# Kernel tuning notes

Measured on AMD Instinct MI355X. Metric: run time of the kernel, lower is better.

## Reference

```python
import jax, jax.numpy as jnp
import numpy as np

B, NBLK, D, DY, NDIM, NMC, DH = 4096, 12, 2, 2, 24, 256, 100
SQRT3 = 3.0 ** 0.5
G2 = np.array([[1.0, 0.0], [0.5, SQRT3 / 2.0]], dtype=np.float32)
G = jnp.asarray(np.kron(np.eye(NBLK, dtype=np.float32), G2))  # (24,24) block-diag hexagonal generator
LOG_VOL = (NDIM // 2) * float(np.log(SQRT3 / 2.0))  # log sqrt(det(G G^T))


def _lin(x, w, b=None):
    y = x @ w.T
    return y if b is None else y + b


def _hex_quantize(y):
    # Exact nearest-point quantizer for the product-of-A2 (hexagonal) lattice.
    p = y.reshape(y.shape[:-1] + (NDIM // 2, 2))
    off = jnp.array([0.5, SQRT3 / 2.0], dtype=y.dtype)
    def rnd(q):  # round to rectangular sublattice Z x sqrt(3)Z
        return jnp.stack([jnp.round(q[..., 0]), jnp.round(q[..., 1] / SQRT3) * SQRT3], axis=-1)
    c0 = rnd(p)
    c1 = rnd(p - off) + off
    d0 = jnp.sum((p - c0) ** 2, axis=-1)
    d1 = jnp.sum((p - c1) ** 2, axis=-1)
    return jnp.where((d0 <= d1)[..., None], c0, c1).reshape(y.shape)


def _logits_cumulative(v, Hs, bs, fs):
    # compressai-style per-channel monotone cumulative network. v: (..., C) -> (..., C)
    v = v[..., None]  # (..., C, 1)
    for k in range(len(Hs)):
        v = jnp.einsum('coi,...ci->...co', jax.nn.softplus(Hs[k]), v) + bs[k][:, :, 0]
        if k < len(fs):
            v = v + jnp.tanh(fs[k][:, :, 0]) * jnp.tanh(v)
    return v[..., 0]


def setup_inputs() -> dict:
    key = jax.random.key(0)
    ks = iter(jax.random.split(key, 64))
    def nrm(shape, s=1.0):
        return jax.random.normal(next(ks), shape, jnp.float32) * s
    inp = {}
    inp['x'] = nrm((B, NBLK, D))
    inp['y_mean'] = nrm((NBLK, DY))
    inp['u'] = jax.random.uniform(next(ks), (NMC, NDIM), jnp.float32)
    inp['ga_w0'] = nrm((DH, D), D ** -0.5); inp['ga_b0'] = jnp.zeros((DH,), jnp.float32)
    inp['ga_w1'] = nrm((DH, DH), DH ** -0.5); inp['ga_b1'] = jnp.zeros((DH,), jnp.float32)
    inp['ga_w2'] = nrm((DY, DH), DH ** -0.5); inp['ga_b2'] = jnp.zeros((DY,), jnp.float32)
    inp['gs_w0'] = nrm((DH, DY), DY ** -0.5); inp['gs_b0'] = jnp.zeros((DH,), jnp.float32)
    inp['gs_w1'] = nrm((DH, DH), DH ** -0.5); inp['gs_b1'] = jnp.zeros((DH,), jnp.float32)
    inp['gs_w2'] = nrm((D, DH), DH ** -0.5); inp['gs_b2'] = jnp.zeros((D,), jnp.float32)
    inp['gac_w0'] = nrm((DH, NDIM), NDIM ** -0.5)
    inp['gac_w1'] = nrm((DH, DH), DH ** -0.5)
    inp['gac_w2'] = nrm((NDIM, DH), DH ** -0.5)
    inp['gsc_w0'] = nrm((DH, NDIM), NDIM ** -0.5)
    inp['gsc_w1'] = nrm((DH, DH), DH ** -0.5)
    inp['gsc_w2'] = nrm((NDIM, DH), DH ** -0.5)
    # factorized-prior cumulative params, layer dims 1->3->3->3->3->1
    inp['eb_H0'] = nrm((NDIM, 3, 1), 0.5)
    inp['eb_H1'] = nrm((NDIM, 3, 3), 0.5)
    inp['eb_H2'] = nrm((NDIM, 3, 3), 0.5)
    inp['eb_H3'] = nrm((NDIM, 3, 3), 0.5)
    inp['eb_H4'] = nrm((NDIM, 1, 3), 0.5)
    inp['eb_b0'] = nrm((NDIM, 3, 1), 0.5)
    inp['eb_b1'] = nrm((NDIM, 3, 1), 0.5)
    inp['eb_b2'] = nrm((NDIM, 3, 1), 0.5)
    inp['eb_b3'] = nrm((NDIM, 3, 1), 0.5)
    inp['eb_b4'] = nrm((NDIM, 1, 1), 0.5)
    inp['eb_a0'] = nrm((NDIM, 3, 1), 0.5)
    inp['eb_a1'] = nrm((NDIM, 3, 1), 0.5)
    inp['eb_a2'] = nrm((NDIM, 3, 1), 0.5)
    inp['eb_a3'] = nrm((NDIM, 3, 1), 0.5)
    return inp


def reference(x, y_mean, u, ga_w0, ga_b0, ga_w1, ga_b1, ga_w2, ga_b2,
              gs_w0, gs_b0, gs_w1, gs_b1, gs_w2, gs_b2,
              gac_w0, gac_w1, gac_w2, gsc_w0, gsc_w1, gsc_w2,
              eb_H0, eb_H1, eb_H2, eb_H3, eb_H4,
              eb_b0, eb_b1, eb_b2, eb_b3, eb_b4,
              eb_a0, eb_a1, eb_a2, eb_a3):
    lrelu, sp = jax.nn.leaky_relu, jax.nn.softplus
    # analysis transform g_a: (B, 12, 2) -> (B, 12, dy)
    y1 = _lin(lrelu(_lin(lrelu(_lin(x, ga_w0, ga_b0)), ga_w1, ga_b1)), ga_w2, ga_b2)
    # EMA zero-mean update (buffer assignment => no gradient through the mean)
    ym = jax.lax.stop_gradient(0.05 * y_mean + 0.95 * jnp.mean(y1, axis=0))
    y1 = (y1 - ym).reshape(B, NDIM)
    # coupled analysis transform g_a_c (Softplus MLP, no bias)
    y1 = _lin(sp(_lin(sp(_lin(y1, gac_w0)), gac_w1)), gac_w2)
    # quasi-uniform samples from the Voronoi cell of the lattice origin
    u2 = u @ G
    u2 = u2 - _hex_quantize(u2)
    # lattice quantization with straight-through estimator
    y_q = _hex_quantize(y1)
    y_hat = y1 + jax.lax.stop_gradient(y_q - y1)
    # Monte-Carlo log-likelihood over the Voronoi cell with factorized prior density
    Hs = (eb_H0, eb_H1, eb_H2, eb_H3, eb_H4)
    bs = (eb_b0, eb_b1, eb_b2, eb_b3, eb_b4)
    fs = (eb_a0, eb_a1, eb_a2, eb_a3)
    pts = y_hat[:, None, :] + u2[None, :, :]  # (B, NMC, NDIM)
    def cdf(p):
        return jax.nn.sigmoid(_logits_cumulative(p, Hs, bs, fs))
    _, pdf = jax.jvp(cdf, (pts,), (jnp.ones_like(pts),))  # density = d/dx cdf(x)
    logp = jnp.sum(jnp.log(pdf + 1e-9), axis=-1)  # (B, NMC)
    lik = jax.scipy.special.logsumexp(logp, axis=1) - jnp.log(jnp.float32(NMC)) + LOG_VOL  # (B,)
    # synthesis transforms
    y_hat1 = _lin(sp(_lin(sp(_lin(y_hat, gsc_w0)), gsc_w1)), gsc_w2).reshape(B, NBLK, DY) + ym
    x_hat = _lin(lrelu(_lin(lrelu(_lin(y_hat1, gs_w0, gs_b0)), gs_w1, gs_b1)), gs_w2, gs_b2)
    return (x_hat, lik)
```

## Files before the change

kernel.cpp:

```cpp
#include <hip/hip_runtime.h>
#include <hip/hip_bf16.h>
#include <math.h>
#include <limits.h>

constexpr int NB    = 4096;
constexpr int ROWS2 = NB * 12;
constexpr int GA_BLOCKS = ROWS2 / 128;
constexpr int TBL_CAP = 64;
constexpr int KBASE   = -32;

constexpr size_t WS_Y1    = 0;
constexpr size_t WS_YHAT  = 98304;
constexpr size_t WS_YHAT1 = 196608;
constexpr size_t WS_YM    = 294912;
constexpr size_t WS_U2T   = 294936;
constexpr size_t WS_EB    = 301080;
constexpr size_t WS_PART  = 302472;
constexpr size_t WS_W1T   = 320904;
constexpr size_t WS_TBL   = 372104;
constexpr size_t WS_END   = WS_TBL + 24 * TBL_CAP * 256;

constexpr float STEP_ODD = 0.8660254037844386f;
constexpr float INV_ODD  = 1.1547005383792517f;

__device__ __forceinline__ float lrelu(float x) { return x >= 0.f ? x : 0.01f * x; }
__device__ __forceinline__ float rcp_fast(float x) { return __builtin_amdgcn_rcpf(x); }

__device__ __forceinline__ float tanh_fast(float x) {
    float xx = fminf(fmaxf(x, -15.f), 15.f);
    float e = __expf(xx + xx);
    return fmaf(-2.f, rcp_fast(e + 1.f), 1.f);
}
__device__ __forceinline__ float splus(float x) {
    return fmaxf(x, 0.f) + __logf(1.f + __expf(-fabsf(x)));
}
__device__ __forceinline__ float splus_precise(float x) {
    return fmaxf(x, 0.f) + log1pf(expf(-fabsf(x)));
}

__device__ __forceinline__ void fma4(float4& a, float h, const float4& w) {
    a.x = fmaf(h, w.x, a.x); a.y = fmaf(h, w.y, a.y);
    a.z = fmaf(h, w.z, a.z); a.w = fmaf(h, w.w, a.w);
}

__device__ __forceinline__ void hexq(float p0, float p1, float& q0, float& q1) {
    const float S3 = 1.7320508075688772f;
    const float H3 = 0.8660254037844386f;
    float c00 = rintf(p0);
    float c01 = rintf(p1 / S3) * S3;
    float c10 = rintf(p0 - 0.5f) + 0.5f;
    float c11 = rintf((p1 - H3) / S3) * S3 + H3;
    float d0 = (p0 - c00) * (p0 - c00) + (p1 - c01) * (p1 - c01);
    float d1 = (p0 - c10) * (p0 - c10) + (p1 - c11) * (p1 - c11);
    bool take0 = d0 <= d1;
    q0 = take0 ? c00 : c10;
    q1 = take0 ? c01 : c11;
}

__device__ __forceinline__ float logpdf_ch(const float* __restrict__ P, float p) {
    float w00 = P[0], w01 = P[1], w02 = P[2];
    float z0 = fmaf(w00, p, P[3]);
    float z1 = fmaf(w01, p, P[4]);
    float z2 = fmaf(w02, p, P[5]);
    float a0 = P[6], a1 = P[7], a2 = P[8];
    float e0 = tanh_fast(z0), e1 = tanh_fast(z1), e2 = tanh_fast(z2);
    float h0 = fmaf(a0, e0, z0), h1 = fmaf(a1, e1, z1), h2 = fmaf(a2, e2, z2);
    float t0 = w00 * fmaf(a0, fmaf(-e0, e0, 1.f), 1.f);
    float t1 = w01 * fmaf(a1, fmaf(-e1, e1, 1.f), 1.f);
    float t2 = w02 * fmaf(a2, fmaf(-e2, e2, 1.f), 1.f);

#define EB_LAYER(O)                                                            \
    {                                                                          \
        float z0n = fmaf(P[O+0], h0, fmaf(P[O+1], h1, fmaf(P[O+2], h2, P[O+9])));  \
        float z1n = fmaf(P[O+3], h0, fmaf(P[O+4], h1, fmaf(P[O+5], h2, P[O+10]))); \
        float z2n = fmaf(P[O+6], h0, fmaf(P[O+7], h1, fmaf(P[O+8], h2, P[O+11]))); \
        float s0 = fmaf(P[O+0], t0, fmaf(P[O+1], t1, P[O+2] * t2));            \
        float s1 = fmaf(P[O+3], t0, fmaf(P[O+4], t1, P[O+5] * t2));            \
        float s2 = fmaf(P[O+6], t0, fmaf(P[O+7], t1, P[O+8] * t2));            \
        float g0 = P[O+12], g1 = P[O+13], g2 = P[O+14];                        \
        float q0 = tanh_fast(z0n), q1 = tanh_fast(z1n), q2 = tanh_fast(z2n);   \
        h0 = fmaf(g0, q0, z0n); h1 = fmaf(g1, q1, z1n); h2 = fmaf(g2, q2, z2n); \
        t0 = s0 * fmaf(g0, fmaf(-q0, q0, 1.f), 1.f);                           \
        t1 = s1 * fmaf(g1, fmaf(-q1, q1, 1.f), 1.f);                           \
        t2 = s2 * fmaf(g2, fmaf(-q2, q2, 1.f), 1.f);                           \
    }
    EB_LAYER(9)
    EB_LAYER(24)
    EB_LAYER(39)
#undef EB_LAYER

    float L = fmaf(P[54], h0, fmaf(P[55], h1, fmaf(P[56], h2, P[57])));
    float T = fmaf(P[54], t0, fmaf(P[55], t1, P[56] * t2));
    float Lc = fminf(fmaxf(L, -30.f), 30.f);
    float sg = rcp_fast(1.f + __expf(-Lc));
    float pdf = sg * (1.f - sg) * T;
    return __logf(pdf + 1e-9f);
}

__global__ __launch_bounds__(256) void k_prep(
    const float* __restrict__ H0p, const float* __restrict__ H1p,
    const float* __restrict__ H2p, const float* __restrict__ H3p,
    const float* __restrict__ H4p,
    const float* __restrict__ b0p, const float* __restrict__ b1p,
    const float* __restrict__ b2p, const float* __restrict__ b3p,
    const float* __restrict__ b4p,
    const float* __restrict__ a0p, const float* __restrict__ a1p,
    const float* __restrict__ a2p, const float* __restrict__ a3p,
    const float* __restrict__ u,
    const float* __restrict__ w1ga, const float* __restrict__ w1gac,
    const float* __restrict__ w1gsc, const float* __restrict__ w1gs,
    float* __restrict__ eb, float* __restrict__ u2t,
    float* __restrict__ w1t)
{
    int tid = threadIdx.x;
    if (blockIdx.x > 0) {
        int t = blockIdx.x - 1;
        int m = t / 50;
        int o = (t % 50) * 256 + tid;
        int k = o >> 7, i = o & 127;
        const float* src = (m == 0) ? w1ga : (m == 1) ? w1gac
                         : (m == 2) ? w1gsc : w1gs;
        w1t[m * 12800 + o] = (i < 100) ? src[i * 100 + k] : 0.f;
        return;
    }
    if (tid < 24) {
        int c = tid;
        float* P = eb + c * 58;
        for (int j = 0; j < 3; ++j) P[j]      = splus_precise(H0p[c*3+j]);
        for (int j = 0; j < 3; ++j) P[3+j]    = b0p[c*3+j];
        for (int j = 0; j < 3; ++j) P[6+j]    = tanhf(a0p[c*3+j]);
        for (int j = 0; j < 9; ++j) P[9+j]    = splus_precise(H1p[c*9+j]);
        for (int j = 0; j < 3; ++j) P[18+j]   = b1p[c*3+j];
        for (int j = 0; j < 3; ++j) P[21+j]   = tanhf(a1p[c*3+j]);
        for (int j = 0; j < 9; ++j) P[24+j]   = splus_precise(H2p[c*9+j]);
        for (int j = 0; j < 3; ++j) P[33+j]   = b2p[c*3+j];
        for (int j = 0; j < 3; ++j) P[36+j]   = tanhf(a2p[c*3+j]);
        for (int j = 0; j < 9; ++j) P[39+j]   = splus_precise(H3p[c*9+j]);
        for (int j = 0; j < 3; ++j) P[48+j]   = b3p[c*3+j];
        for (int j = 0; j < 3; ++j) P[51+j]   = tanhf(a3p[c*3+j]);
        for (int j = 0; j < 3; ++j) P[54+j]   = splus_precise(H4p[c*3+j]);
        P[57] = b4p[c];
    }
    int m = tid;
    if (m < 256) {
        for (int j = 0; j < 12; ++j) {
            float a  = u[m*24 + 2*j];
            float bb = u[m*24 + 2*j + 1];
            float p0 = fmaf(0.5f, bb, a);
            float p1 = 0.8660254037844386f * bb;
            float q0, q1; hexq(p0, p1, q0, q1);
            u2t[(2*j)   * 256 + m] = p0 - q0;
            u2t[(2*j+1) * 256 + m] = p1 - q1;
        }
    }
}

template <int MEAN>
__device__ __forceinline__ void gemm2_body(
    int bid,
    const float* __restrict__ in,
    const float* __restrict__ w0, const float* __restrict__ b0,
    const float* __restrict__ w1t,
    const float* __restrict__ b1, const float* __restrict__ w2,
    const float* __restrict__ b2,
    float* __restrict__ out, float* __restrict__ partial)
{
    __shared__ alignas(16) float shT[100 * 128];
    __shared__ float S[128][2];

    int tid = threadIdx.x;
    int row0 = bid * 128;

    for (int e = tid; e < 12800; e += 256) {
        int j = e >> 7, row = e & 127;
        float2 xv = ((const float2*)in)[row0 + row];
        shT[j * 128 + row] =
            lrelu(fmaf(w0[2*j], xv.x, fmaf(w0[2*j+1], xv.y, b0[j])));
    }

    int rg = tid >> 4;
    int cg = tid & 15;
    __syncthreads();

    float4 acc0[8], acc1[8];
    float4 zero4 = make_float4(0.f, 0.f, 0.f, 0.f);
#pragma unroll
    for (int r = 0; r < 8; ++r) { acc0[r] = zero4; acc1[r] = zero4; }

    const float4* wg = (const float4*)w1t + cg * 2;
    const float4* hp = (const float4*)shT + rg * 2;
    float4 wa0 = wg[0],  wa1 = wg[1];
    float4 wb0 = wg[32], wb1 = wg[33];
#pragma unroll 2
    for (int k = 0; k < 100; ++k) {
        float4 wn0 = wg[(k + 2) * 32];
        float4 wn1 = wg[(k + 2) * 32 + 1];
        float4 ha = hp[k * 32];
        float4 hb = hp[k * 32 + 1];
        fma4(acc0[0], ha.x, wa0); fma4(acc1[0], ha.x, wa1);
        fma4(acc0[1], ha.y, wa0); fma4(acc1[1], ha.y, wa1);
        fma4(acc0[2], ha.z, wa0); fma4(acc1[2], ha.z, wa1);
        fma4(acc0[3], ha.w, wa0); fma4(acc1[3], ha.w, wa1);
        fma4(acc0[4], hb.x, wa0); fma4(acc1[4], hb.x, wa1);
        fma4(acc0[5], hb.y, wa0); fma4(acc1[5], hb.y, wa1);
        fma4(acc0[6], hb.z, wa0); fma4(acc1[6], hb.z, wa1);
        fma4(acc0[7], hb.w, wa0); fma4(acc1[7], hb.w, wa1);
        wa0 = wb0; wa1 = wb1; wb0 = wn0; wb1 = wn1;
    }
    __syncthreads();

    float b1v[8], w20v[8], w21v[8];
    int c0 = cg * 8;
#pragma unroll
    for (int e = 0; e < 8; ++e) {
        int c = c0 + e;
        bool v = (c < 100);
        b1v[e]  = v ? b1[c] : 0.f;
        w20v[e] = v ? w2[c] : 0.f;
        w21v[e] = v ? w2[100 + c] : 0.f;
    }
    float* red = shT;
#pragma unroll
    for (int r = 0; r < 8; ++r) {
        float a0 = lrelu(acc0[r].x + b1v[0]);
        float a1 = lrelu(acc0[r].y + b1v[1]);
        float a2 = lrelu(acc0[r].z + b1v[2]);
        float a3 = lrelu(acc0[r].w + b1v[3]);
        float a4 = lrelu(acc1[r].x + b1v[4]);
        float a5 = lrelu(acc1[r].y + b1v[5]);
        float a6 = lrelu(acc1[r].z + b1v[6]);
        float a7 = lrelu(acc1[r].w + b1v[7]);
        float y0 = a0*w20v[0] + a1*w20v[1] + a2*w20v[2] + a3*w20v[3]
                 + a4*w20v[4] + a5*w20v[5] + a6*w20v[6] + a7*w20v[7];
        float y1 = a0*w21v[0] + a1*w21v[1] + a2*w21v[2] + a3*w21v[3]
                 + a4*w21v[4] + a5*w21v[5] + a6*w21v[6] + a7*w21v[7];
        int row = rg * 8 + r;
        red[(row * 2) * 16 + cg]     = y0;
        red[(row * 2 + 1) * 16 + cg] = y1;
    }
    __syncthreads();
    {
        int row = tid >> 1, p = tid & 1;
        const float4* rp = (const float4*)&red[(row * 2 + p) * 16];
        float4 v0 = rp[0], v1 = rp[1], v2 = rp[2], v3 = rp[3];
        float s = ((v0.x + v0.y) + (v0.z + v0.w))
                + ((v1.x + v1.y) + (v1.z + v1.w))
                + ((v2.x + v2.y) + (v2.z + v2.w))
                + ((v3.x + v3.y) + (v3.z + v3.w));
        float y = s + b2[p];
        out[(row0 + row) * 2 + p] = y;
        if (MEAN) S[row][p] = y;
    }
    if (MEAN) {
        __syncthreads();
        if (tid < 24) {
            int j = tid >> 1, par = tid & 1;
            int base = row0 % 12;
            int k0 = (j - base + 144) % 12;
            float s = 0.f;
            for (int k = k0; k < 128; k += 12) s += S[k][par];
            partial[bid * 24 + tid] = s;
        }
    }
}

__global__ __launch_bounds__(256, 2) void k_ga_table(
    const float* __restrict__ in,
    const float* __restrict__ w0, const float* __restrict__ b0,
    const float* __restrict__ w1t,
    const float* __restrict__ b1, const float* __restrict__ w2,
    const float* __restrict__ b2,
    float* __restrict__ out, float* __restrict__ partial,
    const float* __restrict__ eb, const float* __restrict__ u2t,
    float* __restrict__ tbl)
{
    if (blockIdx.x < (unsigned)GA_BLOCKS) {
        gemm2_body<1>(blockIdx.x, in, w0, b0, w1t, b1, w2, b2, out, partial);
    } else {
        int cv4 = blockIdx.x - GA_BLOCKS;
        int c = cv4 >> 4, vg = (cv4 & 15) * 4;
        int m = threadIdx.x;
        float step = (c & 1) ? STEP_ODD : 0.5f;
        float uv = u2t[c * 256 + m];
        const float* P = eb + c * 58;
#pragma unroll
        for (int dv = 0; dv < 4; ++dv) {
            int v = vg + dv;
            float val = (float)(KBASE + v) * step;
            tbl[(c * TBL_CAP + v) * 256 + m] = logpdf_ch(P, val + uv);
        }
    }
}

__global__ __launch_bounds__(256) void k_mean_final(
    const float* __restrict__ partial, const float* __restrict__ y_mean,
    float* __restrict__ ym)
{
    int tid = threadIdx.x;
    int c = tid >> 3, s = tid & 7;
    float v = 0.f;
    if (c < 24)
        for (int g = s; g < GA_BLOCKS; g += 8) v += partial[g * 24 + c];
    v += __shfl_xor(v, 1); v += __shfl_xor(v, 2); v += __shfl_xor(v, 4);
    if (c < 24 && s == 0)
        ym[c] = fmaf(0.05f, y_mean[c], 0.95f * (v * (1.0f / NB)));
}

__global__ __launch_bounds__(256, 4) void k_fused24(
    const float* __restrict__ y1,
    const float* __restrict__ w0A, const float* __restrict__ w1tA,
    const float* __restrict__ w2A,
    const float* __restrict__ w0B, const float* __restrict__ w1tB,
    const float* __restrict__ w2B,
    const float* __restrict__ ymg,
    float* __restrict__ yhat, float* __restrict__ yhat1)
{
    __shared__ float sw0[2400];
    __shared__ float sw2[2400];
    __shared__ float sX[8 * 25];
    __shared__ float sO[8 * 25];
    __shared__ alignas(16) float h0[100 * 8];
    __shared__ float h1[100 * 8];
    __shared__ float symL[24];

    int tid = threadIdx.x;
    int row0 = blockIdx.x * 8;

    if (tid < 24) symL[tid] = ymg[tid];
    __syncthreads();
    for (int e = tid; e < 192; e += 256) {
        int r = e / 24, c = e - r * 24;
        sX[r * 25 + c] = y1[row0 * 24 + e] - symL[c];
    }

    int ii = tid & 127, rg = tid >> 7;

    for (int pass = 0; pass < 2; ++pass) {
        const float* w0  = pass ? w0B  : w0A;
        const float* w1t = pass ? w1tB : w1tA;
        const float* w2  = pass ? w2B  : w2A;
        for (int t = tid; t < 2400; t += 256) {
            sw0[t] = w0[t];
            sw2[t] = w2[t];
        }
        __syncthreads();

        for (int e = tid; e < 800; e += 256) {
            int j = e >> 3, r = e & 7;
            const float* wr = sw0 + j * 24;
            const float* xr = sX + r * 25;
            float a = 0.f, b = 0.f;
#pragma unroll
            for (int k = 0; k < 24; k += 2) {
                a = fmaf(wr[k],     xr[k],     a);
                b = fmaf(wr[k + 1], xr[k + 1], b);
            }
            h0[j * 8 + r] = splus(a + b);
        }
        __syncthreads();

        {
            float4 a = make_float4(0.f, 0.f, 0.f, 0.f);
            const float* wc = w1t + ii;
            const float4* h4 = (const float4*)h0 + rg;
#pragma unroll 4
            for (int j = 0; j < 100; ++j) {
                float w = wc[j * 128];
                float4 h = h4[j * 2];
                a.x = fmaf(w, h.x, a.x); a.y = fmaf(w, h.y, a.y);
                a.z = fmaf(w, h.z, a.z); a.w = fmaf(w, h.w, a.w);
            }
            if (ii < 100) {
                h1[ii * 8 + rg * 4]     = splus(a.x);
                h1[ii * 8 + rg * 4 + 1] = splus(a.y);
                h1[ii * 8 + rg * 4 + 2] = splus(a.z);
                h1[ii * 8 + rg * 4 + 3] = splus(a.w);
            }
        }
        __syncthreads();

        if (tid < 192) {
            int c = tid >> 3, r = tid & 7;
            const float* w2r = sw2 + c * 100;
            float s = 0.f, s2 = 0.f;
#pragma unroll 4
            for (int i = 0; i < 100; i += 2) {
                s  = fmaf(w2r[i],     h1[i * 8 + r],       s);
                s2 = fmaf(w2r[i + 1], h1[(i + 1) * 8 + r], s2);
            }
            float v = s + s2;
            if (pass == 0) sO[r * 25 + c] = v;
            else yhat1[(row0 + r) * 24 + c] = v + symL[c];
        }

        if (pass == 0) {
            __syncthreads();
            if (tid < 96) {
                int pr = tid >> 3, r = tid & 7;
                float v0 = sO[r * 25 + 2*pr], v1 = sO[r * 25 + 2*pr + 1];
                float q0, q1; hexq(v0, v1, q0, q1);
                yhat[(row0 + r) * 24 + 2*pr]     = q0;
                yhat[(row0 + r) * 24 + 2*pr + 1] = q1;
                sX[r * 25 + 2*pr]     = q0;
                sX[r * 25 + 2*pr + 1] = q1;
            }
        }
    }
}

__global__ __launch_bounds__(256, 2) void k_gs_mc(
    const float* __restrict__ yhat1,
    const float* __restrict__ w0, const float* __restrict__ b0,
    const float* __restrict__ w1t,
    const float* __restrict__ b1, const float* __restrict__ w2,
    const float* __restrict__ b2, float* __restrict__ xhat,
    const float* __restrict__ yhat, const float* __restrict__ u2t,
    const float* __restrict__ eb,
    const float* __restrict__ tbl, float* __restrict__ lik)
{
    if (blockIdx.x < (unsigned)GA_BLOCKS) {
        gemm2_body<0>(blockIdx.x, yhat1, w0, b0, w1t, b1, w2, b2, xhat, nullptr);
        return;
    }
    __shared__ float sy[4 * 24];
    __shared__ float redm[4], reds[4];
    int tid = threadIdx.x;
    int wv = tid >> 6;
    int bg = (blockIdx.x - GA_BLOCKS) * 4;

    if (tid < 96) sy[tid] = yhat[bg * 24 + tid];
    __syncthreads();

    for (int q = 0; q < 4; ++q) {
        float lp = 0.f;
        unsigned miss = 0;
#pragma unroll
        for (int c = 0; c < 24; ++c) {
            float yv = sy[q * 24 + c];
            float inv = (c & 1) ? INV_ODD : 2.0f;
            int k = (int)rintf(yv * inv);
            int idx = k - KBASE;
            bool ok = (idx >= 0 && idx < TBL_CAP);
            int idq = min(max(idx, 0), TBL_CAP - 1);
            float tv = tbl[(c * TBL_CAP + idq) * 256 + tid];
            lp += ok ? tv : 0.f;
            if (!ok) miss |= (1u << c);
        }
        while (miss) {
            int c = __ffs(miss) - 1;
            miss &= miss - 1;
            lp += logpdf_ch(eb + c * 58, sy[q * 24 + c] + u2t[c * 256 + tid]);
        }

        float m = lp;
#pragma unroll
        for (int off = 1; off < 64; off <<= 1) m = fmaxf(m, __shfl_xor(m, off));
        if ((tid & 63) == 0) redm[wv] = m;
        __syncthreads();
        float mx = fmaxf(fmaxf(redm[0], redm[1]), fmaxf(redm[2], redm[3]));
        float e = __expf(lp - mx);
#pragma unroll
        for (int off = 1; off < 64; off <<= 1) e += __shfl_xor(e, off);
        if ((tid & 63) == 0) reds[wv] = e;
        __syncthreads();
        if (tid == 0)
            lik[bg + q] = mx + __logf(reds[0] + reds[1] + reds[2] + reds[3])
                        - 7.271269879190247f;
        __syncthreads();
    }
}

__global__ __launch_bounds__(256, 2) void k_gs(
    const float* __restrict__ yhat1,
    const float* __restrict__ w0, const float* __restrict__ b0,
    const float* __restrict__ w1t,
    const float* __restrict__ b1, const float* __restrict__ w2,
    const float* __restrict__ b2, float* __restrict__ xhat)
{
    gemm2_body<0>(blockIdx.x, yhat1, w0, b0, w1t, b1, w2, b2, xhat, nullptr);
}

__global__ __launch_bounds__(256) void k_mc_direct(
    const float* __restrict__ yhat, const float* __restrict__ u2t,
    const float* __restrict__ eb, float* __restrict__ lik)
{
    __shared__ alignas(16) float sU[24 * 256];
    __shared__ float redm[4], reds[4];
    int tid = threadIdx.x;
    int wv = tid >> 6;
    int b = blockIdx.x;
    for (int i = tid; i < 1536; i += 256)
        ((float4*)sU)[i] = ((const float4*)u2t)[i];
    __syncthreads();

    float lp = 0.f;
    for (int c = 0; c < 24; ++c)
        lp += logpdf_ch(eb + c * 58, yhat[b * 24 + c] + sU[c * 256 + tid]);

    float m = lp;
#pragma unroll
    for (int off = 1; off < 64; off <<= 1) m = fmaxf(m, __shfl_xor(m, off));
    if ((tid & 63) == 0) redm[wv] = m;
    __syncthreads();
    float mx = fmaxf(fmaxf(redm[0], redm[1]), fmaxf(redm[2], redm[3]));
    float e = __expf(lp - mx);
#pragma unroll
    for (int off = 1; off < 64; off <<= 1) e += __shfl_xor(e, off);
    if ((tid & 63) == 0) reds[wv] = e;
    __syncthreads();
    if (tid == 0)
        lik[b] = mx + __logf(reds[0] + reds[1] + reds[2] + reds[3])
               - 7.271269879190247f;
}

extern "C" void kernel_launch(void* const* d_in, const int* in_sizes, int n_in,
                              void* d_out, int out_size, void* d_ws, size_t ws_size,
                              hipStream_t stream)
{
    (void)in_sizes; (void)n_in; (void)out_size;
    const float* x      = (const float*)d_in[0];
    const float* y_mean = (const float*)d_in[1];
    const float* u      = (const float*)d_in[2];
    const float* ga_w0  = (const float*)d_in[3];
    const float* ga_b0  = (const float*)d_in[4];
    const float* ga_w1  = (const float*)d_in[5];
    const float* ga_b1  = (const float*)d_in[6];
    const float* ga_w2  = (const float*)d_in[7];
    const float* ga_b2  = (const float*)d_in[8];
    const float* gs_w0  = (const float*)d_in[9];
    const float* gs_b0  = (const float*)d_in[10];
    const float* gs_w1  = (const float*)d_in[11];
    const float* gs_b1  = (const float*)d_in[12];
    const float* gs_w2  = (const float*)d_in[13];
    const float* gs_b2  = (const float*)d_in[14];
    const float* gac_w0 = (const float*)d_in[15];
    const float* gac_w1 = (const float*)d_in[16];
    const float* gac_w2 = (const float*)d_in[17];
    const float* gsc_w0 = (const float*)d_in[18];
    const float* gsc_w1 = (const float*)d_in[19];
    const float* gsc_w2 = (const float*)d_in[20];
    const float* eb_H0  = (const float*)d_in[21];
    const float* eb_H1  = (const float*)d_in[22];
    const float* eb_H2  = (const float*)d_in[23];
    const float* eb_H3  = (const float*)d_in[24];
    const float* eb_H4  = (const float*)d_in[25];
    const float* eb_b0  = (const float*)d_in[26];
    const float* eb_b1  = (const float*)d_in[27];
    const float* eb_b2  = (const float*)d_in[28];
    const float* eb_b3  = (const float*)d_in[29];
    const float* eb_b4  = (const float*)d_in[30];
    const float* eb_a0  = (const float*)d_in[31];
    const float* eb_a1  = (const float*)d_in[32];
    const float* eb_a2  = (const float*)d_in[33];
    const float* eb_a3  = (const float*)d_in[34];

    float* ws    = (float*)d_ws;
    float* y1    = ws + WS_Y1;
    float* yhat  = ws + WS_YHAT;
    float* yhat1 = ws + WS_YHAT1;
    float* ym    = ws + WS_YM;
    float* u2t   = ws + WS_U2T;
    float* eb    = ws + WS_EB;
    float* part  = ws + WS_PART;
    float* w1t   = ws + WS_W1T;
    float* tbl   = ws + WS_TBL;
    float* xhat  = (float*)d_out;
    float* lik   = (float*)d_out + 98304;

    float* w1tGA  = w1t;
    float* w1tGAC = w1t + 12800;
    float* w1tGSC = w1t + 25600;
    float* w1tGS  = w1t + 38400;

    bool use_tbl = ws_size >= WS_END * sizeof(float);

    k_prep<<<201, 256, 0, stream>>>(eb_H0, eb_H1, eb_H2, eb_H3, eb_H4,
                                    eb_b0, eb_b1, eb_b2, eb_b3, eb_b4,
                                    eb_a0, eb_a1, eb_a2, eb_a3, u,
                                    ga_w1, gac_w1, gsc_w1, gs_w1,
                                    eb, u2t, w1t);
    if (use_tbl)
        k_ga_table<<<GA_BLOCKS + 24 * TBL_CAP / 4, 256, 0, stream>>>(
            x, ga_w0, ga_b0, w1tGA, ga_b1, ga_w2, ga_b2, y1, part,
            eb, u2t, tbl);
    else
        k_ga_table<<<GA_BLOCKS, 256, 0, stream>>>(
            x, ga_w0, ga_b0, w1tGA, ga_b1, ga_w2, ga_b2, y1, part,
            eb, u2t, tbl);
    k_mean_final<<<1, 256, 0, stream>>>(part, y_mean, ym);
    k_fused24<<<NB / 8, 256, 0, stream>>>(y1, gac_w0, w1tGAC, gac_w2,
                                          gsc_w0, w1tGSC, gsc_w2,
                                          ym, yhat, yhat1);
    if (use_tbl) {
        k_gs_mc<<<GA_BLOCKS + NB / 4, 256, 0, stream>>>(
            yhat1, gs_w0, gs_b0, w1tGS, gs_b1, gs_w2, gs_b2, xhat,
            yhat, u2t, eb, tbl, lik);
    } else {
        k_gs<<<GA_BLOCKS, 256, 0, stream>>>(
            yhat1, gs_w0, gs_b0, w1tGS, gs_b1, gs_w2, gs_b2, xhat);
        k_mc_direct<<<NB, 256, 0, stream>>>(yhat, u2t, eb, lik);
    }
}
```

Measured before the change: 122.2 us.

## Replace shared-memory tiled 2-D MLP GEMM with per-thread register dot products

The 2→100→100→2 MLP body (ga and gs) no longer stages the hidden layer in shared memory and runs a register-tiled outer-product GEMM. Each thread now keeps its row's 100 hidden activations in registers and computes dot products against the untransposed w1 rows, split across two wave-pairs that each handle half the outputs, reduced through a small shared buffer. This drops the transpose prep for ga_w1 and gs_w1, so k_prep launches fewer blocks. The trade-off is heavy register pressure from h[100], which risks spills or lower occupancy. Each thread also rereads wave-uniform weights from global/scalar memory, and per-thread FLOPs now exceed the shared-tile reuse scheme.

```diff
diff --git a/kernel.cpp b/kernel.cpp
--- a/kernel.cpp
+++ b/kernel.cpp
@@ -36,11 +36,6 @@
 }
 __device__ __forceinline__ float splus_precise(float x) {
     return fmaxf(x, 0.f) + log1pf(expf(-fabsf(x)));
-}
-
-__device__ __forceinline__ void fma4(float4& a, float h, const float4& w) {
-    a.x = fmaf(h, w.x, a.x); a.y = fmaf(h, w.y, a.y);
-    a.z = fmaf(h, w.z, a.z); a.w = fmaf(h, w.w, a.w);
 }
 
 __device__ __forceinline__ void hexq(float p0, float p1, float& q0, float& q1) {
@@ -107,8 +102,7 @@
     const float* __restrict__ a0p, const float* __restrict__ a1p,
     const float* __restrict__ a2p, const float* __restrict__ a3p,
     const float* __restrict__ u,
-    const float* __restrict__ w1ga, const float* __restrict__ w1gac,
-    const float* __restrict__ w1gsc, const float* __restrict__ w1gs,
+    const float* __restrict__ w1gac, const float* __restrict__ w1gsc,
     float* __restrict__ eb, float* __restrict__ u2t,
     float* __restrict__ w1t)
 {
@@ -118,8 +112,7 @@
         int m = t / 50;
         int o = (t % 50) * 256 + tid;
         int k = o >> 7, i = o & 127;
-        const float* src = (m == 0) ? w1ga : (m == 1) ? w1gac
-                         : (m == 2) ? w1gsc : w1gs;
+        const float* src = (m == 0) ? w1gac : w1gsc;
         w1t[m * 12800 + o] = (i < 100) ? src[i * 100 + k] : 0.f;
         return;
     }
@@ -160,96 +153,57 @@
     int bid,
     const float* __restrict__ in,
     const float* __restrict__ w0, const float* __restrict__ b0,
-    const float* __restrict__ w1t,
+    const float* __restrict__ w1,
     const float* __restrict__ b1, const float* __restrict__ w2,
     const float* __restrict__ b2,
     float* __restrict__ out, float* __restrict__ partial)
 {
-    __shared__ alignas(16) float shT[100 * 128];
+    __shared__ float S2[128][2][2];
     __shared__ float S[128][2];
 
     int tid = threadIdx.x;
+    int lane = tid & 63;
+    int wv = tid >> 6;
+    int half = wv >> 1;
+    int rsub = (wv & 1) * 64;
+    int lrow = rsub + lane;
     int row0 = bid * 128;
 
-    for (int e = tid; e < 12800; e += 256) {
-        int j = e >> 7, row = e & 127;
-        float2 xv = ((const float2*)in)[row0 + row];
-        shT[j * 128 + row] =
-            lrelu(fmaf(w0[2*j], xv.x, fmaf(w0[2*j+1], xv.y, b0[j])));
-    }
-
-    int rg = tid >> 4;
-    int cg = tid & 15;
+    float2 xv = ((const float2*)in)[row0 + lrow];
+
+    float h[100];
+#pragma unroll
+    for (int j = 0; j < 100; ++j)
+        h[j] = lrelu(fmaf(w0[2*j], xv.x, fmaf(w0[2*j+1], xv.y, b0[j])));
+
+    float y0 = 0.f, y1 = 0.f;
+    const float* w1h = w1 + half * 50 * 100;
+    const float* b1h = b1 + half * 50;
+    const float* w2h0 = w2 + half * 50;
+    const float* w2h1 = w2 + 100 + half * 50;
+    for (int ii = 0; ii < 50; ++ii) {
+        const float* wr = w1h + ii * 100;
+        float s0 = 0.f, s1 = 0.f, s2 = 0.f, s3 = 0.f;
+#pragma unroll
+        for (int j = 0; j < 100; j += 4) {
+            s0 = fmaf(wr[j],     h[j],     s0);
+            s1 = fmaf(wr[j + 1], h[j + 1], s1);
+            s2 = fmaf(wr[j + 2], h[j + 2], s2);
+            s3 = fmaf(wr[j + 3], h[j + 3], s3);
+        }
+        float a = lrelu(((s0 + s1) + (s2 + s3)) + b1h[ii]);
+        y0 = fmaf(w2h0[ii], a, y0);
+        y1 = fmaf(w2h1[ii], a, y1);
+    }
+    S2[lrow][half][0] = y0;
+    S2[lrow][half][1] = y1;
     __syncthreads();
 
-    float4 acc0[8], acc1[8];
-    float4 zero4 = make_float4(0.f, 0.f, 0.f, 0.f);
-#pragma unroll
-    for (int r = 0; r < 8; ++r) { acc0[r] = zero4; acc1[r] = zero4; }
-
-    const float4* wg = (const float4*)w1t + cg * 2;
-    const float4* hp = (const float4*)shT + rg * 2;
-    float4 wa0 = wg[0],  wa1 = wg[1];
-    float4 wb0 = wg[32], wb1 = wg[33];
-#pragma unroll 2
-    for (int k = 0; k < 100; ++k) {
-        float4 wn0 = wg[(k + 2) * 32];
-        float4 wn1 = wg[(k + 2) * 32 + 1];
-        float4 ha = hp[k * 32];
-        float4 hb = hp[k * 32 + 1];
-        fma4(acc0[0], ha.x, wa0); fma4(acc1[0], ha.x, wa1);
-        fma4(acc0[1], ha.y, wa0); fma4(acc1[1], ha.y, wa1);
-        fma4(acc0[2], ha.z, wa0); fma4(acc1[2], ha.z, wa1);
-        fma4(acc0[3], ha.w, wa0); fma4(acc1[3], ha.w, wa1);
-        fma4(acc0[4], hb.x, wa0); fma4(acc1[4], hb.x, wa1);
-        fma4(acc0[5], hb.y, wa0); fma4(acc1[5], hb.y, wa1);
-        fma4(acc0[6], hb.z, wa0); fma4(acc1[6], hb.z, wa1);
-        fma4(acc0[7], hb.w, wa0); fma4(acc1[7], hb.w, wa1);
-        wa0 = wb0; wa1 = wb1; wb0 = wn0; wb1 = wn1;
-    }
-    __syncthreads();
-
-    float b1v[8], w20v[8], w21v[8];
-    int c0 = cg * 8;
-#pragma unroll
-    for (int e = 0; e < 8; ++e) {
-        int c = c0 + e;
-        bool v = (c < 100);
-        b1v[e]  = v ? b1[c] : 0.f;
-        w20v[e] = v ? w2[c] : 0.f;
-        w21v[e] = v ? w2[100 + c] : 0.f;
-    }
-    float* red = shT;
-#pragma unroll
-    for (int r = 0; r < 8; ++r) {
-        float a0 = lrelu(acc0[r].x + b1v[0]);
-        float a1 = lrelu(acc0[r].y + b1v[1]);
-        float a2 = lrelu(acc0[r].z + b1v[2]);
-        float a3 = lrelu(acc0[r].w + b1v[3]);
-        float a4 = lrelu(acc1[r].x + b1v[4]);
-        float a5 = lrelu(acc1[r].y + b1v[5]);
-        float a6 = lrelu(acc1[r].z + b1v[6]);
-        float a7 = lrelu(acc1[r].w + b1v[7]);
-        float y0 = a0*w20v[0] + a1*w20v[1] + a2*w20v[2] + a3*w20v[3]
-                 + a4*w20v[4] + a5*w20v[5] + a6*w20v[6] + a7*w20v[7];
-        float y1 = a0*w21v[0] + a1*w21v[1] + a2*w21v[2] + a3*w21v[3]
-                 + a4*w21v[4] + a5*w21v[5] + a6*w21v[6] + a7*w21v[7];
-        int row = rg * 8 + r;
-        red[(row * 2) * 16 + cg]     = y0;
-        red[(row * 2 + 1) * 16 + cg] = y1;
-    }
-    __syncthreads();
     {
-        int row = tid >> 1, p = tid & 1;
-        const float4* rp = (const float4*)&red[(row * 2 + p) * 16];
-        float4 v0 = rp[0], v1 = rp[1], v2 = rp[2], v3 = rp[3];
-        float s = ((v0.x + v0.y) + (v0.z + v0.w))
-                + ((v1.x + v1.y) + (v1.z + v1.w))
-                + ((v2.x + v2.y) + (v2.z + v2.w))
-                + ((v3.x + v3.y) + (v3.z + v3.w));
-        float y = s + b2[p];
-        out[(row0 + row) * 2 + p] = y;
-        if (MEAN) S[row][p] = y;
+        int r = tid >> 1, p = tid & 1;
+        float y = (S2[r][0][p] + S2[r][1][p]) + b2[p];
+        out[(row0 + r) * 2 + p] = y;
+        if (MEAN) S[r][p] = y;
     }
     if (MEAN) {
         __syncthreads();
@@ -267,7 +221,7 @@
 __global__ __launch_bounds__(256, 2) void k_ga_table(
     const float* __restrict__ in,
     const float* __restrict__ w0, const float* __restrict__ b0,
-    const float* __restrict__ w1t,
+    const float* __restrict__ w1,
     const float* __restrict__ b1, const float* __restrict__ w2,
     const float* __restrict__ b2,
     float* __restrict__ out, float* __restrict__ partial,
@@ -275,7 +229,7 @@
     float* __restrict__ tbl)
 {
     if (blockIdx.x < (unsigned)GA_BLOCKS) {
-        gemm2_body<1>(blockIdx.x, in, w0, b0, w1t, b1, w2, b2, out, partial);
+        gemm2_body<1>(blockIdx.x, in, w0, b0, w1, b1, w2, b2, out, partial);
     } else {
         int cv4 = blockIdx.x - GA_BLOCKS;
         int c = cv4 >> 4, vg = (cv4 & 15) * 4;
@@ -411,7 +365,7 @@
 __global__ __launch_bounds__(256, 2) void k_gs_mc(
     const float* __restrict__ yhat1,
     const float* __restrict__ w0, const float* __restrict__ b0,
-    const float* __restrict__ w1t,
+    const float* __restrict__ w1,
     const float* __restrict__ b1, const float* __restrict__ w2,
     const float* __restrict__ b2, float* __restrict__ xhat,
     const float* __restrict__ yhat, const float* __restrict__ u2t,
@@ -419,7 +373,7 @@
     const float* __restrict__ tbl, float* __restrict__ lik)
 {
     if (blockIdx.x < (unsigned)GA_BLOCKS) {
-        gemm2_body<0>(blockIdx.x, yhat1, w0, b0, w1t, b1, w2, b2, xhat, nullptr);
+        gemm2_body<0>(blockIdx.x, yhat1, w0, b0, w1, b1, w2, b2, xhat, nullptr);
         return;
     }
     __shared__ float sy[4 * 24];
@@ -473,11 +427,11 @@
 __global__ __launch_bounds__(256, 2) void k_gs(
     const float* __restrict__ yhat1,
     const float* __restrict__ w0, const float* __restrict__ b0,
-    const float* __restrict__ w1t,
+    const float* __restrict__ w1,
     const float* __restrict__ b1, const float* __restrict__ w2,
     const float* __restrict__ b2, float* __restrict__ xhat)
 {
-    gemm2_body<0>(blockIdx.x, yhat1, w0, b0, w1t, b1, w2, b2, xhat, nullptr);
+    gemm2_body<0>(blockIdx.x, yhat1, w0, b0, w1, b1, w2, b2, xhat, nullptr);
 }
 
 __global__ __launch_bounds__(256) void k_mc_direct(
@@ -567,25 +521,22 @@
     float* xhat  = (float*)d_out;
     float* lik   = (float*)d_out + 98304;
 
-    float* w1tGA  = w1t;
-    float* w1tGAC = w1t + 12800;
-    float* w1tGSC = w1t + 25600;
-    float* w1tGS  = w1t + 38400;
+    float* w1tGAC = w1t;
+    float* w1tGSC = w1t + 12800;
 
     bool use_tbl = ws_size >= WS_END * sizeof(float);
 
-    k_prep<<<201, 256, 0, stream>>>(eb_H0, eb_H1, eb_H2, eb_H3, eb_H4,
+    k_prep<<<101, 256, 0, stream>>>(eb_H0, eb_H1, eb_H2, eb_H3, eb_H4,
                                     eb_b0, eb_b1, eb_b2, eb_b3, eb_b4,
                                     eb_a0, eb_a1, eb_a2, eb_a3, u,
-                                    ga_w1, gac_w1, gsc_w1, gs_w1,
-                                    eb, u2t, w1t);
+                                    gac_w1, gsc_w1, eb, u2t, w1t);
     if (use_tbl)
         k_ga_table<<<GA_BLOCKS + 24 * TBL_CAP / 4, 256, 0, stream>>>(
-            x, ga_w0, ga_b0, w1tGA, ga_b1, ga_w2, ga_b2, y1, part,
+            x, ga_w0, ga_b0, ga_w1, ga_b1, ga_w2, ga_b2, y1, part,
             eb, u2t, tbl);
     else
         k_ga_table<<<GA_BLOCKS, 256, 0, stream>>>(
-            x, ga_w0, ga_b0, w1tGA, ga_b1, ga_w2, ga_b2, y1, part,
+            x, ga_w0, ga_b0, ga_w1, ga_b1, ga_w2, ga_b2, y1, part,
             eb, u2t, tbl);
     k_mean_final<<<1, 256, 0, stream>>>(part, y_mean, ym);
     k_fused24<<<NB / 8, 256, 0, stream>>>(y1, gac_w0, w1tGAC, gac_w2,
@@ -593,11 +544,11 @@
                                           ym, yhat, yhat1);
     if (use_tbl) {
         k_gs_mc<<<GA_BLOCKS + NB / 4, 256, 0, stream>>>(
-            yhat1, gs_w0, gs_b0, w1tGS, gs_b1, gs_w2, gs_b2, xhat,
+            yhat1, gs_w0, gs_b0, gs_w1, gs_b1, gs_w2, gs_b2, xhat,
             yhat, u2t, eb, tbl, lik);
     } else {
         k_gs<<<GA_BLOCKS, 256, 0, stream>>>(
-            yhat1, gs_w0, gs_b0, w1tGS, gs_b1, gs_w2, gs_b2, xhat);
+            yhat1, gs_w0, gs_b0, gs_w1, gs_b1, gs_w2, gs_b2, xhat);
         k_mc_direct<<<NB, 256, 0, stream>>>(yhat, u2t, eb, lik);
     }
 }
```

Measured after the change: 249.6 us. 2.04x slower.

## Run the gs synthesis MLP hidden layer on bf16 MFMA instructions

Applied to the files above, without the earlier changes.

Replaces the fp32 scalar 100x100 hidden-layer GEMM in the final synthesis transform with a bf16 MFMA 16x16x32 path. The layer-0 activations are built directly into register A-fragments, and the transposed weight is pre-converted to bf16 in the prep kernel. Each wave handles 16 rows, and the block count doubles to 64 rows per block with a higher occupancy launch bound. This trades fp32 precision of x_hat for matrix-core throughput, which may affect tolerance.

```diff
diff --git a/kernel.cpp b/kernel.cpp
--- a/kernel.cpp
+++ b/kernel.cpp
@@ -6,6 +6,7 @@
 constexpr int NB    = 4096;
 constexpr int ROWS2 = NB * 12;
 constexpr int GA_BLOCKS = ROWS2 / 128;
+constexpr int GS_BLOCKS = ROWS2 / 64;
 constexpr int TBL_CAP = 64;
 constexpr int KBASE   = -32;
 
@@ -17,14 +18,24 @@
 constexpr size_t WS_EB    = 301080;
 constexpr size_t WS_PART  = 302472;
 constexpr size_t WS_W1T   = 320904;
-constexpr size_t WS_TBL   = 372104;
+constexpr size_t WS_W1BF  = 359304;
+constexpr size_t WS_TBL   = 366472;
 constexpr size_t WS_END   = WS_TBL + 24 * TBL_CAP * 256;
 
 constexpr float STEP_ODD = 0.8660254037844386f;
 constexpr float INV_ODD  = 1.1547005383792517f;
 
+typedef __attribute__((ext_vector_type(8))) short bf16x8;
+typedef __attribute__((ext_vector_type(4))) float f32x4;
+
 __device__ __forceinline__ float lrelu(float x) { return x >= 0.f ? x : 0.01f * x; }
 __device__ __forceinline__ float rcp_fast(float x) { return __builtin_amdgcn_rcpf(x); }
+
+__device__ __forceinline__ unsigned short f2bf(float f) {
+    unsigned b = __float_as_uint(f);
+    b += 0x7FFFu + ((b >> 16) & 1u);
+    return (unsigned short)(b >> 16);
+}
 
 __device__ __forceinline__ float tanh_fast(float x) {
     float xx = fminf(fmaxf(x, -15.f), 15.f);
@@ -110,17 +121,23 @@
     const float* __restrict__ w1ga, const float* __restrict__ w1gac,
     const float* __restrict__ w1gsc, const float* __restrict__ w1gs,
     float* __restrict__ eb, float* __restrict__ u2t,
-    float* __restrict__ w1t)
+    float* __restrict__ w1t, float* __restrict__ w1bf)
 {
     int tid = threadIdx.x;
     if (blockIdx.x > 0) {
         int t = blockIdx.x - 1;
-        int m = t / 50;
-        int o = (t % 50) * 256 + tid;
-        int k = o >> 7, i = o & 127;
-        const float* src = (m == 0) ? w1ga : (m == 1) ? w1gac
-                         : (m == 2) ? w1gsc : w1gs;
-        w1t[m * 12800 + o] = (i < 100) ? src[i * 100 + k] : 0.f;
+        if (t < 150) {
+            int m = t / 50;
+            int o = (t % 50) * 256 + tid;
+            int k = o >> 7, i = o & 127;
+            const float* src = (m == 0) ? w1ga : (m == 1) ? w1gac : w1gsc;
+            w1t[m * 12800 + o] = (i < 100) ? src[i * 100 + k] : 0.f;
+        } else {
+            int o = (t - 150) * 256 + tid;
+            int i = o >> 7, k = o & 127;
+            float v = (i < 100 && k < 100) ? w1gs[i * 100 + k] : 0.f;
+            ((unsigned short*)w1bf)[o] = f2bf(v);
+        }
         return;
     }
     if (tid < 24) {
@@ -264,6 +281,84 @@
     }
 }
 
+__device__ __forceinline__ void gs_mfma_body(
+    int bid,
+    const float* __restrict__ in,
+    const float* __restrict__ w0, const float* __restrict__ b0,
+    const float* __restrict__ w1bf,
+    const float* __restrict__ b1, const float* __restrict__ w2,
+    const float* __restrict__ b2,
+    float* __restrict__ out)
+{
+    int tid = threadIdx.x;
+    int lane = tid & 63, wv = tid >> 6;
+    int rsel = lane & 15;
+    int kgrp = lane >> 4;
+    int row0w = bid * 64 + wv * 16;
+
+    float2 xv = ((const float2*)in)[row0w + rsel];
+
+    bf16x8 afr[4];
+#pragma unroll
+    for (int kb = 0; kb < 4; ++kb) {
+#pragma unroll
+        for (int j8 = 0; j8 < 8; ++j8) {
+            int j = kb * 32 + kgrp * 8 + j8;
+            float h = 0.f;
+            if (j < 100)
+                h = lrelu(fmaf(w0[2*j], xv.x, fmaf(w0[2*j+1], xv.y, b0[j])));
+            afr[kb][j8] = (short)f2bf(h);
+        }
+    }
+
+    const unsigned short* w1u = (const unsigned short*)w1bf;
+    f32x4 acc[7];
+#pragma unroll
+    for (int n = 0; n < 7; ++n) acc[n] = (f32x4){0.f, 0.f, 0.f, 0.f};
+#pragma unroll
+    for (int kb = 0; kb < 4; ++kb) {
+#pragma unroll
+        for (int n = 0; n < 7; ++n) {
+            bf16x8 bfr = *(const bf16x8*)(w1u + (n * 16 + rsel) * 128
+                                              + kb * 32 + kgrp * 8);
+            acc[n] = __builtin_amdgcn_mfma_f32_16x16x32_bf16(afr[kb], bfr,
+                                                             acc[n], 0, 0, 0);
+        }
+    }
+
+    float py0[4] = {0.f, 0.f, 0.f, 0.f}, py1[4] = {0.f, 0.f, 0.f, 0.f};
+#pragma unroll
+    for (int n = 0; n < 7; ++n) {
+        int i = n * 16 + rsel;
+        bool v = (i < 100);
+        float b1v = v ? b1[i] : 0.f;
+        float w20 = v ? w2[i] : 0.f;
+        float w21 = v ? w2[100 + i] : 0.f;
+#pragma unroll
+        for (int r = 0; r < 4; ++r) {
+            float a = lrelu(acc[n][r] + b1v);
+            py0[r] = fmaf(a, w20, py0[r]);
+            py1[r] = fmaf(a, w21, py1[r]);
+        }
+    }
+#pragma unroll
+    for (int r = 0; r < 4; ++r) {
+#pragma unroll
+        for (int off = 1; off < 16; off <<= 1) {
+            py0[r] += __shfl_xor(py0[r], off);
+            py1[r] += __shfl_xor(py1[r], off);
+        }
+    }
+    if (rsel == 0) {
+#pragma unroll
+        for (int r = 0; r < 4; ++r) {
+            int row = row0w + kgrp * 4 + r;
+            out[row * 2]     = py0[r] + b2[0];
+            out[row * 2 + 1] = py1[r] + b2[1];
+        }
+    }
+}
+
 __global__ __launch_bounds__(256, 2) void k_ga_table(
     const float* __restrict__ in,
     const float* __restrict__ w0, const float* __restrict__ b0,
@@ -408,25 +503,25 @@
     }
 }
 
-__global__ __launch_bounds__(256, 2) void k_gs_mc(
+__global__ __launch_bounds__(256, 4) void k_gs_mc(
     const float* __restrict__ yhat1,
     const float* __restrict__ w0, const float* __restrict__ b0,
-    const float* __restrict__ w1t,
+    const float* __restrict__ w1bf,
     const float* __restrict__ b1, const float* __restrict__ w2,
     const float* __restrict__ b2, float* __restrict__ xhat,
     const float* __restrict__ yhat, const float* __restrict__ u2t,
     const float* __restrict__ eb,
     const float* __restrict__ tbl, float* __restrict__ lik)
 {
-    if (blockIdx.x < (unsigned)GA_BLOCKS) {
-        gemm2_body<0>(blockIdx.x, yhat1, w0, b0, w1t, b1, w2, b2, xhat, nullptr);
+    if (blockIdx.x < (unsigned)GS_BLOCKS) {
+        gs_mfma_body(blockIdx.x, yhat1, w0, b0, w1bf, b1, w2, b2, xhat);
         return;
     }
     __shared__ float sy[4 * 24];
     __shared__ float redm[4], reds[4];
     int tid = threadIdx.x;
     int wv = tid >> 6;
-    int bg = (blockIdx.x - GA_BLOCKS) * 4;
+    int bg = (blockIdx.x - GS_BLOCKS) * 4;
 
     if (tid < 96) sy[tid] = yhat[bg * 24 + tid];
     __syncthreads();
@@ -470,14 +565,14 @@
     }
 }
 
-__global__ __launch_bounds__(256, 2) void k_gs(
+__global__ __launch_bounds__(256, 4) void k_gs(
     const float* __restrict__ yhat1,
     const float* __restrict__ w0, const float* __restrict__ b0,
-    const float* __restrict__ w1t,
+    const float* __restrict__ w1bf,
     const float* __restrict__ b1, const float* __restrict__ w2,
     const float* __restrict__ b2, float* __restrict__ xhat)
 {
-    gemm2_body<0>(blockIdx.x, yhat1, w0, b0, w1t, b1, w2, b2, xhat, nullptr);
+    gs_mfma_body(blockIdx.x, yhat1, w0, b0, w1bf, b1, w2, b2, xhat);
 }
 
 __global__ __launch_bounds__(256) void k_mc_direct(
@@ -563,6 +658,7 @@
     float* eb    = ws + WS_EB;
     float* part  = ws + WS_PART;
     float* w1t   = ws + WS_W1T;
+    float* w1bf  = ws + WS_W1BF;
     float* tbl   = ws + WS_TBL;
     float* xhat  = (float*)d_out;
     float* lik   = (float*)d_out + 98304;
@@ -570,15 +666,14 @@
     float* w1tGA  = w1t;
     float* w1tGAC = w1t + 12800;
     float* w1tGSC = w1t + 25600;
-    float* w1tGS  = w1t + 38400;
 
     bool use_tbl = ws_size >= WS_END * sizeof(float);
 
-    k_prep<<<201, 256, 0, stream>>>(eb_H0, eb_H1, eb_H2, eb_H3, eb_H4,
+    k_prep<<<207, 256, 0, stream>>>(eb_H0, eb_H1, eb_H2, eb_H3, eb_H4,
                                     eb_b0, eb_b1, eb_b2, eb_b3, eb_b4,
                                     eb_a0, eb_a1, eb_a2, eb_a3, u,
                                     ga_w1, gac_w1, gsc_w1, gs_w1,
-                                    eb, u2t, w1t);
+                                    eb, u2t, w1t, w1bf);
     if (use_tbl)
         k_ga_table<<<GA_BLOCKS + 24 * TBL_CAP / 4, 256, 0, stream>>>(
             x, ga_w0, ga_b0, w1tGA, ga_b1, ga_w2, ga_b2, y1, part,
@@ -592,12 +687,12 @@
                                           gsc_w0, w1tGSC, gsc_w2,
                                           ym, yhat, yhat1);
     if (use_tbl) {
-        k_gs_mc<<<GA_BLOCKS + NB / 4, 256, 0, stream>>>(
-            yhat1, gs_w0, gs_b0, w1tGS, gs_b1, gs_w2, gs_b2, xhat,
+        k_gs_mc<<<GS_BLOCKS + NB / 4, 256, 0, stream>>>(
+            yhat1, gs_w0, gs_b0, w1bf, gs_b1, gs_w2, gs_b2, xhat,
             yhat, u2t, eb, tbl, lik);
     } else {
-        k_gs<<<GA_BLOCKS, 256, 0, stream>>>(
-            yhat1, gs_w0, gs_b0, w1tGS, gs_b1, gs_w2, gs_b2, xhat);
+        k_gs<<<GS_BLOCKS, 256, 0, stream>>>(
+            yhat1, gs_w0, gs_b0, w1bf, gs_b1, gs_w2, gs_b2, xhat);
         k_mc_direct<<<NB, 256, 0, stream>>>(yhat, u2t, eb, lik);
     }
 }
```

Measured after the change: 113.6 us, median of 2. -7.1%, faster.
